# Performance work log

Measured on AMD Instinct MI355X. Metric: run time of the kernel, lower is better.

The kernel has to match this reference:

```python
import jax, jax.numpy as jnp
import numpy as np

# LCA hyperparameters (from init_kwargs)
NUM_LATENT = 2048
NUM_STEPS = 100
STEP_SIZE = 0.01
SPARSE_MULT = 0.3
# thresh_type='soft', rectify_a=True -> rectified soft threshold


def lca_threshold(u):
    # rectified soft threshold: a = relu(u - lambda)
    return jax.nn.relu(u - SPARSE_MULT)


def setup_inputs() -> dict:
    key = jax.random.key(0)
    kx, kw = jax.random.split(key)
    x = jax.random.normal(kx, (8192, 784), dtype=jnp.float32)
    w = jax.random.normal(kw, (784, NUM_LATENT), dtype=jnp.float32)
    # normalize dictionary columns (standard LCA practice; keeps the
    # fixed-point iteration u <- u + s*(b - a@G - u) numerically stable)
    w = w / jnp.linalg.norm(w, axis=0, keepdims=True)
    return {"x": x, "w": w}


def reference(x, w):
    # x: [B, 784], w: [784, L]
    x = x.reshape(-1, 28 * 28)
    b = x @ w                                        # excitatory current [B, L]
    g = w.T @ w - jnp.eye(NUM_LATENT, dtype=w.dtype)  # inhibitory connectivity [L, L]

    u0 = jnp.zeros((x.shape[0], NUM_LATENT), dtype=x.dtype)
    a0 = lca_threshold(u0)

    def step(carry, _):
        u, a = carry
        du = b - a @ g - u
        u_new = u + STEP_SIZE * du
        a_new = lca_threshold(u_new)
        return (u_new, a_new), None

    # original runs num_steps-1 updates after the initial state
    (u, a), _ = jax.lax.scan(step, (u0, a0), None, length=NUM_STEPS - 1)

    reconstruction = a @ w.T  # [B, 784]
    return (reconstruction, a)
```

## Files before the change

kernel.cpp:

```cpp
#include <hip/hip_runtime.h>
#include <hip/hip_bf16.h>
#include <stdint.h>


typedef __bf16 bf16_t;
typedef float f32x4 __attribute__((ext_vector_type(4)));
typedef __bf16 bf16x8 __attribute__((ext_vector_type(8)));
typedef int int4v __attribute__((ext_vector_type(4)));

#define BM 128
#define BK 32

static __device__ __forceinline__ f32x4 mfma16(int4v a, int4v b, f32x4 c) {
    return __builtin_amdgcn_mfma_f32_16x16x32_bf16(
        __builtin_bit_cast(bf16x8, a), __builtin_bit_cast(bf16x8, b), c, 0, 0, 0);
}

static __device__ __forceinline__ void gl_lds16(const bf16_t* gp, bf16_t* lp) {
    auto g1 = (const __attribute__((address_space(1))) uint32_t*)(uintptr_t)gp;
    auto l3 = (__attribute__((address_space(3))) uint32_t*)(uintptr_t)lp;
    __builtin_amdgcn_global_load_lds(g1, l3, 16, 0, 0);
}

__global__ void sniff(const uint16_t* __restrict__ wh, int* __restrict__ flag) {
    __shared__ int cnt;
    if (threadIdx.x == 0) cnt = 0;
    __syncthreads();
    int c = 0;
    for (int t = threadIdx.x; t < 4096; t += 256) {
        uint16_t h = wh[(size_t)2 * t * 97];
        c += (((h >> 7) & 0xFF) >= 0x82);
    }
    atomicAdd(&cnt, c);
    __syncthreads();
    if (threadIdx.x == 0) flag[0] = (cnt > 256) ? 1 : 0;
}

__global__ void fill0(int4v* __restrict__ p, long n16) {
    long i = (long)blockIdx.x * 256 + threadIdx.x;
    if (i < n16) p[i] = (int4v){0, 0, 0, 0};
}

__global__ void build_w(const void* __restrict__ w, bf16_t* __restrict__ wT,
                        bf16_t* __restrict__ wB, const int* __restrict__ flag) {
    const int k = blockIdx.x * 256 + threadIdx.x;
    const int j = blockIdx.y;
    if (k >= 800) return;
    bf16_t v = (bf16_t)0.0f;
    if (k < 784) {
        v = flag[0] ? (bf16_t)((const float*)w)[(size_t)k * 2048 + j]
                    : ((const bf16_t*)w)[(size_t)k * 2048 + j];
        wB[(size_t)k * 2048 + j] = v;
    }
    wT[(size_t)j * 800 + k] = v;
}

template <int MODE, bool CLAMPN, int BNT>
__global__ __launch_bounds__(256, 2) void gemm_nt(
    const bf16_t* __restrict__ A, const bf16_t* __restrict__ B,
    int N, int K, int lda, int ldb,
    const void* __restrict__ Xin, float* __restrict__ U,
    bf16_t* __restrict__ Out, int ldo, const int* __restrict__ flag)
{
    constexpr int NTC = BNT / 32;
    __shared__ __align__(16) bf16_t sA[BM * BK];
    __shared__ __align__(16) bf16_t sB[BNT * BK];

    const int tid  = threadIdx.x;
    const int lane = tid & 63;
    const int wave = tid >> 6;
    const int wm   = wave >> 1;
    const int wn   = wave & 1;
    const int bm   = blockIdx.x * BM;
    const int bn   = blockIdx.y * BNT;

    f32x4 acc[4][NTC];
#pragma unroll
    for (int i = 0; i < 4; ++i)
#pragma unroll
        for (int j = 0; j < NTC; ++j) acc[i][j] = (f32x4){0.f, 0.f, 0.f, 0.f};

    const int s_row = tid >> 2;
    const int s_cc  = tid & 3;

    int rB0 = bn + s_row;
    int rB1 = bn + 64 + s_row;
    if (CLAMPN) { rB0 = min(rB0, N - 1); rB1 = min(rB1, N - 1); }
    const bf16_t* gA0 = A + (size_t)(bm + s_row) * lda + s_cc * 8;
    const bf16_t* gA1 = A + (size_t)(bm + 64 + s_row) * lda + s_cc * 8;
    const bf16_t* gB0 = B + (size_t)rB0 * ldb + s_cc * 8;
    const bf16_t* gB1 = B + (size_t)rB1 * ldb + s_cc * 8;

    bf16_t* dA0 = sA + (size_t)tid * 8;
    bf16_t* dA1 = sA + (size_t)(256 + tid) * 8;
    bf16_t* dB0 = sB + (size_t)tid * 8;
    bf16_t* dB1 = sB + (size_t)(256 + tid) * 8;

    const int mrow = lane & 15;
    const int q    = lane >> 4;

    for (int k0 = 0; k0 < K; k0 += BK) {
        gl_lds16(gA0 + k0, dA0);
        gl_lds16(gA1 + k0, dA1);
        gl_lds16(gB0 + k0, dB0);
        if constexpr (BNT == 128) gl_lds16(gB1 + k0, dB1);
        __syncthreads();

        int4v af[4], bf[NTC];
        const bf16_t* pa = sA + ((wm * 64 + mrow) * BK + q * 8);
        const bf16_t* pb = sB + ((wn * (BNT / 2) + mrow) * BK + q * 8);
#pragma unroll
        for (int t = 0; t < 4; ++t) af[t] = *(const int4v*)(pa + t * 16 * BK);
#pragma unroll
        for (int t = 0; t < NTC; ++t) bf[t] = *(const int4v*)(pb + t * 16 * BK);
#pragma unroll
        for (int mt = 0; mt < 4; ++mt)
#pragma unroll
            for (int nt = 0; nt < NTC; ++nt)
                acc[mt][nt] = mfma16(af[mt], bf[nt], acc[mt][nt]);
        __syncthreads();
    }

    int f = 0;
    if (MODE == 0) f = flag[0];

    const int coln = lane & 15;
    const int rq   = lane >> 4;
#pragma unroll
    for (int mt = 0; mt < 4; ++mt) {
#pragma unroll
        for (int r = 0; r < 4; ++r) {
            const int gm = bm + wm * 64 + mt * 16 + rq * 4 + r;
#pragma unroll
            for (int nt = 0; nt < NTC; ++nt) {
                const int gn = bn + wn * (BNT / 2) + nt * 16 + coln;
                const float c = acc[mt][nt][r];
                if (MODE == 0) {
                    if (gn < N) {
                        const size_t xi = (size_t)gm * N + gn;
                        const float xv = f ? ((const float*)Xin)[xi]
                                           : (float)((const bf16_t*)Xin)[xi];
                        Out[(size_t)gm * ldo + gn] = (bf16_t)(xv - c);
                    }
                } else if (MODE == 1) {
                    const size_t idx = (size_t)gm * ldo + gn;
                    const float uo = U[idx];
                    const float ao = fmaxf(uo - 0.3f, 0.0f);
                    const float un = uo + 0.01f * (c + ao - uo);
                    U[idx] = un;
                    Out[idx] = (bf16_t)fmaxf(un - 0.3f, 0.0f);
                } else {
                    if (gn < N)
                        Out[(size_t)gm * ldo + gn] = (bf16_t)c;
                }
            }
        }
    }
}

__global__ void a_move(const bf16_t* __restrict__ src, float* __restrict__ dst,
                       long lo, long hi, const int* __restrict__ flag) {
    if (!flag[0]) return;
    long i = lo + (long)blockIdx.x * 256 + threadIdx.x;
    if (i < hi) dst[i] = (float)src[i];
}

__global__ void recon_out(const bf16_t* __restrict__ rec, void* __restrict__ dout,
                          const int* __restrict__ flag) {
    long i = (long)blockIdx.x * 256 + threadIdx.x;
    if (i >= 6422528L) return;
    if (flag[0]) ((float*)dout)[i] = (float)rec[i];
    else         ((bf16_t*)dout)[i] = rec[i];
}

extern "C" void kernel_launch(void* const* d_in, const int* in_sizes, int n_in,
                              void* d_out, int out_size, void* d_ws, size_t ws_size,
                              hipStream_t stream) {
    const void* x = d_in[0];
    const void* w = d_in[1];
    (void)in_sizes; (void)n_in; (void)out_size; (void)ws_size;

    char* ws = (char*)d_ws;
    float*  u    = (float*)ws;
    bf16_t* r    = (bf16_t*)(ws + 67108864);
    bf16_t* wT   = (bf16_t*)(ws + 80216064);
    bf16_t* wB   = (bf16_t*)(ws + 83492864);
    int*    flag = (int*)(ws + 86704128);
    bf16_t* aA   = (bf16_t*)((char*)d_out + 12845056);
    bf16_t* rec  = r;

    sniff<<<1, 256, 0, stream>>>((const uint16_t*)w, flag);
    fill0<<<16384, 256, 0, stream>>>((int4v*)u, 4194304L);
    fill0<<<3200, 256, 0, stream>>>((int4v*)r, 819200L);
    fill0<<<8192, 256, 0, stream>>>((int4v*)aA, 2097152L);
    build_w<<<dim3(4, 2048), 256, 0, stream>>>(w, wT, wB, flag);

    for (int i = 0; i < 99; ++i) {
        gemm_nt<0, true, 64><<<dim3(64, 13), 256, 0, stream>>>(
            aA, wB, 784, 2048, 2048, 2048, x, nullptr, r, 800, flag);
        gemm_nt<1, false, 128><<<dim3(64, 16), 256, 0, stream>>>(
            r, wT, 2048, 800, 800, 800, nullptr, u, aA, 2048, flag);
    }

    gemm_nt<2, true, 64><<<dim3(64, 13), 256, 0, stream>>>(
        aA, wB, 784, 2048, 2048, 2048, nullptr, nullptr, rec, 784, flag);

    float* aOutF = (float*)d_out + 6422528;
    a_move<<<45312, 256, 0, stream>>>(aA, aOutF, 5177344L, 16777216L, flag);
    a_move<<<20224, 256, 0, stream>>>(aA, aOutF, 0L, 5177344L, flag);

    recon_out<<<25088, 256, 0, stream>>>(rec, d_out, flag);
}
```

Baseline: 10.09 ms.

## Double-buffer LDS tiles with async prefetch and deeper K tile in GEMMs

The GEMM kernel now keeps two LDS buffers. While the current K tile is being multiplied, it issues the global_load_lds prefetch for the next tile, and explicit vmcnt waits gate the hand-off to that buffer. The K tile size becomes a template parameter: the a@w GEMMs use 64 and the r@wT GEMM keeps 32. This is meant to hide global memory latency that was fully exposed by the old load-sync-compute loop. In exchange, LDS use doubles, and correctness now depends on hand-written waitcnt values matching the number of loads issued per stage.

Result: slower. 11.33 ms (+12.3%).

```diff
diff --git a/kernel.cpp b/kernel.cpp
--- a/kernel.cpp
+++ b/kernel.cpp
@@ -9,7 +9,6 @@
 typedef int int4v __attribute__((ext_vector_type(4)));
 
 #define BM 128
-#define BK 32
 
 static __device__ __forceinline__ f32x4 mfma16(int4v a, int4v b, f32x4 c) {
     return __builtin_amdgcn_mfma_f32_16x16x32_bf16(
@@ -20,6 +19,14 @@
     auto g1 = (const __attribute__((address_space(1))) uint32_t*)(uintptr_t)gp;
     auto l3 = (__attribute__((address_space(3))) uint32_t*)(uintptr_t)lp;
     __builtin_amdgcn_global_load_lds(g1, l3, 16, 0, 0);
+}
+
+template <int N>
+static __device__ __forceinline__ void vm_wait() {
+    if constexpr (N == 0)      asm volatile("s_waitcnt vmcnt(0)" ::: "memory");
+    else if constexpr (N == 4) asm volatile("s_waitcnt vmcnt(4)" ::: "memory");
+    else if constexpr (N == 6) asm volatile("s_waitcnt vmcnt(6)" ::: "memory");
+    else                       static_assert(N == 0, "unsupported vmcnt");
 }
 
 __global__ void sniff(const uint16_t* __restrict__ wh, int* __restrict__ flag) {
@@ -55,7 +62,7 @@
     wT[(size_t)j * 800 + k] = v;
 }
 
-template <int MODE, bool CLAMPN, int BNT>
+template <int MODE, bool CLAMPN, int BNT, int TBK>
 __global__ __launch_bounds__(256, 2) void gemm_nt(
     const bf16_t* __restrict__ A, const bf16_t* __restrict__ B,
     int N, int K, int lda, int ldb,
@@ -63,8 +70,14 @@
     bf16_t* __restrict__ Out, int ldo, const int* __restrict__ flag)
 {
     constexpr int NTC = BNT / 32;
-    __shared__ __align__(16) bf16_t sA[BM * BK];
-    __shared__ __align__(16) bf16_t sB[BNT * BK];
+    constexpr int CPR = TBK / 8;
+    constexpr int AL  = BM * CPR / 256;
+    constexpr int BL  = BNT * CPR / 256;
+    constexpr int L   = AL + BL;
+    constexpr int KH  = TBK / 32;
+
+    __shared__ __align__(16) bf16_t sA[2][BM * TBK];
+    __shared__ __align__(16) bf16_t sB[2][BNT * TBK];
 
     const int tid  = threadIdx.x;
     const int lane = tid & 63;
@@ -80,45 +93,69 @@
 #pragma unroll
         for (int j = 0; j < NTC; ++j) acc[i][j] = (f32x4){0.f, 0.f, 0.f, 0.f};
 
-    const int s_row = tid >> 2;
-    const int s_cc  = tid & 3;
-
-    int rB0 = bn + s_row;
-    int rB1 = bn + 64 + s_row;
-    if (CLAMPN) { rB0 = min(rB0, N - 1); rB1 = min(rB1, N - 1); }
-    const bf16_t* gA0 = A + (size_t)(bm + s_row) * lda + s_cc * 8;
-    const bf16_t* gA1 = A + (size_t)(bm + 64 + s_row) * lda + s_cc * 8;
-    const bf16_t* gB0 = B + (size_t)rB0 * ldb + s_cc * 8;
-    const bf16_t* gB1 = B + (size_t)rB1 * ldb + s_cc * 8;
-
-    bf16_t* dA0 = sA + (size_t)tid * 8;
-    bf16_t* dA1 = sA + (size_t)(256 + tid) * 8;
-    bf16_t* dB0 = sB + (size_t)tid * 8;
-    bf16_t* dB1 = sB + (size_t)(256 + tid) * 8;
+    const bf16_t* gA[AL];
+    const bf16_t* gB[BL];
+#pragma unroll
+    for (int l = 0; l < AL; ++l) {
+        const int c = l * 256 + tid;
+        gA[l] = A + (size_t)(bm + c / CPR) * lda + (c & (CPR - 1)) * 8;
+    }
+#pragma unroll
+    for (int l = 0; l < BL; ++l) {
+        const int c = l * 256 + tid;
+        int rb = bn + c / CPR;
+        if (CLAMPN) rb = min(rb, N - 1);
+        gB[l] = B + (size_t)rb * ldb + (c & (CPR - 1)) * 8;
+    }
+
+    auto stage = [&](int buf, int k0) {
+#pragma unroll
+        for (int l = 0; l < AL; ++l)
+            gl_lds16(gA[l] + k0, &sA[buf][(size_t)(l * 256 + tid) * 8]);
+#pragma unroll
+        for (int l = 0; l < BL; ++l)
+            gl_lds16(gB[l] + k0, &sB[buf][(size_t)(l * 256 + tid) * 8]);
+    };
 
     const int mrow = lane & 15;
     const int q    = lane >> 4;
 
-    for (int k0 = 0; k0 < K; k0 += BK) {
-        gl_lds16(gA0 + k0, dA0);
-        gl_lds16(gA1 + k0, dA1);
-        gl_lds16(gB0 + k0, dB0);
-        if constexpr (BNT == 128) gl_lds16(gB1 + k0, dB1);
-        __syncthreads();
-
-        int4v af[4], bf[NTC];
-        const bf16_t* pa = sA + ((wm * 64 + mrow) * BK + q * 8);
-        const bf16_t* pb = sB + ((wn * (BNT / 2) + mrow) * BK + q * 8);
-#pragma unroll
-        for (int t = 0; t < 4; ++t) af[t] = *(const int4v*)(pa + t * 16 * BK);
-#pragma unroll
-        for (int t = 0; t < NTC; ++t) bf[t] = *(const int4v*)(pb + t * 16 * BK);
-#pragma unroll
-        for (int mt = 0; mt < 4; ++mt)
-#pragma unroll
-            for (int nt = 0; nt < NTC; ++nt)
-                acc[mt][nt] = mfma16(af[mt], bf[nt], acc[mt][nt]);
-        __syncthreads();
+    stage(0, 0);
+    int cur = 0;
+    for (int k0 = 0; k0 < K; k0 += TBK) {
+        if (k0 + TBK < K) {
+            stage(cur ^ 1, k0 + TBK);
+            vm_wait<L>();
+        } else {
+            vm_wait<0>();
+        }
+        __builtin_amdgcn_s_barrier();
+        asm volatile("" ::: "memory");
+
+        int4v af[4][KH], bv[NTC][KH];
+        const bf16_t* pa = &sA[cur][(wm * 64 + mrow) * TBK + q * 8];
+        const bf16_t* pb = &sB[cur][(wn * (BNT / 2) + mrow) * TBK + q * 8];
+#pragma unroll
+        for (int t = 0; t < 4; ++t)
+#pragma unroll
+            for (int kk = 0; kk < KH; ++kk)
+                af[t][kk] = *(const int4v*)(pa + t * 16 * TBK + kk * 32);
+#pragma unroll
+        for (int t = 0; t < NTC; ++t)
+#pragma unroll
+            for (int kk = 0; kk < KH; ++kk)
+                bv[t][kk] = *(const int4v*)(pb + t * 16 * TBK + kk * 32);
+#pragma unroll
+        for (int kk = 0; kk < KH; ++kk)
+#pragma unroll
+            for (int mt = 0; mt < 4; ++mt)
+#pragma unroll
+                for (int nt = 0; nt < NTC; ++nt)
+                    acc[mt][nt] = mfma16(af[mt][kk], bv[nt][kk], acc[mt][nt]);
+
+        asm volatile("s_waitcnt lgkmcnt(0)" ::: "memory");
+        __builtin_amdgcn_s_barrier();
+        cur ^= 1;
     }
 
     int f = 0;
@@ -196,13 +233,13 @@
     build_w<<<dim3(4, 2048), 256, 0, stream>>>(w, wT, wB, flag);
 
     for (int i = 0; i < 99; ++i) {
-        gemm_nt<0, true, 64><<<dim3(64, 13), 256, 0, stream>>>(
+        gemm_nt<0, true, 64, 64><<<dim3(64, 13), 256, 0, stream>>>(
             aA, wB, 784, 2048, 2048, 2048, x, nullptr, r, 800, flag);
-        gemm_nt<1, false, 128><<<dim3(64, 16), 256, 0, stream>>>(
+        gemm_nt<1, false, 128, 32><<<dim3(64, 16), 256, 0, stream>>>(
             r, wT, 2048, 800, 800, 800, nullptr, u, aA, 2048, flag);
     }
 
-    gemm_nt<2, true, 64><<<dim3(64, 13), 256, 0, stream>>>(
+    gemm_nt<2, true, 64, 64><<<dim3(64, 13), 256, 0, stream>>>(
         aA, wB, 784, 2048, 2048, 2048, nullptr, nullptr, rec, 784, flag);
 
     float* aOutF = (float*)d_out + 6422528;
```
